# Performance work log

Measured on AMD Instinct MI355X. Metric: run time of the kernel, lower is better.

The kernel has to match this reference:

```python
import jax, jax.numpy as jnp
import numpy as np

N_LAYERS = 2
D_MODEL = 1024
D_INNER = 2 * D_MODEL
D_STATE = 16
D_CONV = 4
DT_RANK = D_MODEL // 16  # 64
B_SZ, L = 1, 2048
EPS = 1e-5


def layernorm(x, w, b):
    mu = jnp.mean(x, axis=-1, keepdims=True)
    var = jnp.mean(jnp.square(x - mu), axis=-1, keepdims=True)
    return (x - mu) * jax.lax.rsqrt(var + EPS) * w + b


def mamba(x, in_w, cw, cb, xp_w, dtp_w, dtp_b, A_log, Dp, out_w):
    # x: [B, L, D_MODEL]
    Bn, Ln, _ = x.shape
    xz = jnp.einsum('bld,ed->ble', x, in_w)          # [B,L,2*D_INNER]
    xc, z = jnp.split(xz, 2, axis=-1)
    # causal depthwise conv1d (kernel D_CONV)
    xp = jnp.pad(xc, ((0, 0), (D_CONV - 1, 0), (0, 0)))
    xc = sum(xp[:, k:k + Ln, :] * cw[:, k] for k in range(D_CONV)) + cb
    xc = jax.nn.silu(xc)
    dbl = jnp.einsum('ble,re->blr', xc, xp_w)        # [B,L,DT_RANK+2*D_STATE]
    dt, Bm, Cm = jnp.split(dbl, [DT_RANK, DT_RANK + D_STATE], axis=-1)
    dt = jax.nn.softplus(jnp.einsum('blr,er->ble', dt, dtp_w) + dtp_b)  # [B,L,E]
    A = -jnp.exp(A_log)                              # [E,N], strictly negative
    dA = jnp.exp(dt[..., None] * A)                  # [B,L,E,N]
    dBu = (dt * xc)[..., None] * Bm[:, :, None, :]   # [B,L,E,N]

    def step(h, inp):
        dA_t, dBu_t, C_t = inp
        h = dA_t * h + dBu_t                         # [B,E,N]
        y = jnp.einsum('ben,bn->be', h, C_t)
        return h, y

    h0 = jnp.zeros((Bn, D_INNER, D_STATE), dA.dtype)
    _, ys = jax.lax.scan(step, h0, (dA.transpose(1, 0, 2, 3),
                                    dBu.transpose(1, 0, 2, 3),
                                    Cm.transpose(1, 0, 2)))
    y = ys.transpose(1, 0, 2) + xc * Dp              # [B,L,E]
    y = y * jax.nn.silu(z)
    return jnp.einsum('ble,de->bld', y, out_w)       # [B,L,D_MODEL]


def setup_inputs() -> dict:
    key = jax.random.key(0)
    ks = jax.random.split(key, 12)
    s = 0.02
    dt_init = np.log(np.expm1(0.01)).astype(np.float32)  # softplus^-1(0.01)
    A_row = jnp.log(jnp.arange(1, D_STATE + 1, dtype=jnp.float32))
    return {
        'x': jax.random.normal(ks[0], (B_SZ, L, D_MODEL), jnp.float32),
        'ln_w': jnp.ones((N_LAYERS, D_MODEL), jnp.float32),
        'ln_b': jnp.zeros((N_LAYERS, D_MODEL), jnp.float32),
        'in_proj_w': jax.random.normal(ks[1], (N_LAYERS, 2 * D_INNER, D_MODEL)) * s,
        'conv_w': jax.random.normal(ks[2], (N_LAYERS, D_INNER, D_CONV)) * 0.2,
        'conv_b': jnp.zeros((N_LAYERS, D_INNER), jnp.float32),
        'x_proj_w': jax.random.normal(ks[3], (N_LAYERS, DT_RANK + 2 * D_STATE, D_INNER)) * s,
        'dt_proj_w': jax.random.normal(ks[4], (N_LAYERS, D_INNER, DT_RANK)) * (DT_RANK ** -0.5),
        'dt_proj_b': jnp.full((N_LAYERS, D_INNER), dt_init),
        'A_log': jnp.broadcast_to(A_row, (N_LAYERS, D_INNER, D_STATE)).copy(),
        'D_skip': jnp.ones((N_LAYERS, D_INNER), jnp.float32),
        'out_proj_w': jax.random.normal(ks[5], (N_LAYERS, D_MODEL, D_INNER)) * s,
        'norm_f_w': jnp.ones((D_MODEL,), jnp.float32),
        'norm_f_b': jnp.zeros((D_MODEL,), jnp.float32),
    }


def reference(x, ln_w, ln_b, in_proj_w, conv_w, conv_b, x_proj_w, dt_proj_w,
              dt_proj_b, A_log, D_skip, out_proj_w, norm_f_w, norm_f_b):
    for i in range(N_LAYERS):
        h = layernorm(x, ln_w[i], ln_b[i])
        h = mamba(h, in_proj_w[i], conv_w[i], conv_b[i], x_proj_w[i],
                  dt_proj_w[i], dt_proj_b[i], A_log[i], D_skip[i], out_proj_w[i])
        x = h + x  # residual (dropout/drop_path are identity in eval)
    return layernorm(x, norm_f_w, norm_f_b)
```

## Files before the change

### kernel.cpp

```cpp
#include <hip/hip_runtime.h>
#include <hip/hip_bf16.h>
#include <math.h>

#define LSEQ 2048
#define DMODEL 1024
#define DINNER 2048
#define DSTATE 16
#define DCONV 4
#define DTRANK 64
#define RPROJ 96

#define CHUNK 16
#define NCHUNK (LSEQ / CHUNK)

#define XSPLIT 4

typedef __attribute__((ext_vector_type(8))) short bf16x8;
typedef __attribute__((ext_vector_type(4))) float f32x4;

__device__ __forceinline__ float softplusf(float x) {
    return (x > 20.f) ? x : log1pf(__expf(x));
}
__device__ __forceinline__ float siluf(float x) {
    return x / (1.f + __expf(-x));
}
__device__ __forceinline__ short f2bf(float f) {
    union { float f; unsigned u; } v; v.f = f;
    unsigned r = v.u + 0x7FFFu + ((v.u >> 16) & 1u);
    return (short)(r >> 16);
}
__device__ __forceinline__ float bf2f(short h) {
    union { unsigned u; float f; } v;
    v.u = ((unsigned)(unsigned short)h) << 16;
    return v.f;
}

__device__ __forceinline__ void cvt8(const float* __restrict__ s,
                                     short* __restrict__ d, int i) {
    const float4 a = *(const float4*)(s + i);
    const float4 b = *(const float4*)(s + i + 4);
    alignas(16) short h[8];
    h[0] = f2bf(a.x); h[1] = f2bf(a.y); h[2] = f2bf(a.z); h[3] = f2bf(a.w);
    h[4] = f2bf(b.x); h[5] = f2bf(b.y); h[6] = f2bf(b.z); h[7] = f2bf(b.w);
    *(uint4*)(d + i) = *(const uint4*)h;
}

__global__ __launch_bounds__(256) void cvt_weights(
    const float* __restrict__ s0, short* __restrict__ d0, int n0,
    const float* __restrict__ s1, short* __restrict__ d1, int n1,
    const float* __restrict__ s2, short* __restrict__ d2, int n2,
    const float* __restrict__ s3, short* __restrict__ d3, int n3)
{
    int i = (blockIdx.x * 256 + threadIdx.x) * 8;
    if (i < n0) { cvt8(s0, d0, i); return; }
    i -= n0;
    if (i < n1) { cvt8(s1, d1, i); return; }
    i -= n1;
    if (i < n2) { cvt8(s2, d2, i); return; }
    i -= n2;
    if (i < n3) { cvt8(s3, d3, i); return; }
}

__global__ __launch_bounds__(256) void ln_kernel(
    const float* __restrict__ x, const float* __restrict__ w,
    const float* __restrict__ b, float* __restrict__ outf,
    short* __restrict__ outb)
{
    __shared__ float s1[256], s2[256];
    const int row = blockIdx.x;
    const int tid = threadIdx.x;
    const float* xr = x + (size_t)row * DMODEL;
    float v[4];
    float s = 0.f, sq = 0.f;
#pragma unroll
    for (int k = 0; k < 4; k++) {
        v[k] = xr[k * 256 + tid];
        s += v[k];
        sq += v[k] * v[k];
    }
    s1[tid] = s; s2[tid] = sq;
    __syncthreads();
    for (int off = 128; off > 0; off >>= 1) {
        if (tid < off) { s1[tid] += s1[tid + off]; s2[tid] += s2[tid + off]; }
        __syncthreads();
    }
    const float mu = s1[0] * (1.f / DMODEL);
    const float var = s2[0] * (1.f / DMODEL) - mu * mu;
    const float rstd = rsqrtf(var + 1e-5f);
#pragma unroll
    for (int k = 0; k < 4; k++) {
        const int i = k * 256 + tid;
        const float o = (v[k] - mu) * rstd * w[i] + b[i];
        if (outf) outf[(size_t)row * DMODEL + i] = o;
        if (outb) outb[(size_t)row * DMODEL + i] = f2bf(o);
    }
}

template<int MI, int NJ, int MODE>
__global__ __launch_bounds__(256) void gemm_mfma(
    const short* __restrict__ A, int lda,
    const short* __restrict__ W, int ldw,
    float* __restrict__ Cf, short* __restrict__ Cb, int ldc,
    int M, int N, int K,
    const float* __restrict__ resid)
{
    constexpr int BM = 32 * MI;
    constexpr int BN = 32 * NJ;
    constexpr int AISS = BM / 64;
    constexpr int WISS = BN / 64;
    __shared__ alignas(16) short As[BM * 32];
    __shared__ alignas(16) short Ws[BN * 32];

    const int tid = threadIdx.x;
    const int lane = tid & 63;
    const int w = tid >> 6;
    const int wr = w >> 1, wc = w & 1;
    const int row0 = blockIdx.y * BM;
    const int col0 = blockIdx.x * BN;
    const int kbeg = blockIdx.z * K;

    const int srow = tid >> 2;
    const int skch = ((tid & 3) ^ ((srow >> 1) & 3)) * 8;

    f32x4 acc[MI][NJ];
#pragma unroll
    for (int i = 0; i < MI; i++)
#pragma unroll
        for (int j = 0; j < NJ; j++) acc[i][j] = (f32x4)0.f;

    const int lrow = lane & 15;
    const int q = lane >> 4;

    for (int kt = kbeg; kt < kbeg + K; kt += 32) {
        __syncthreads();
#pragma unroll
        for (int j = 0; j < AISS; j++) {
            const short* gp = A + (size_t)(row0 + j * 64 + srow) * lda + kt + skch;
            __builtin_amdgcn_global_load_lds(
                (const __attribute__((address_space(1))) void*)gp,
                (__attribute__((address_space(3))) void*)(&As[j * 2048 + tid * 8]),
                16, 0, 0);
        }
#pragma unroll
        for (int j = 0; j < WISS; j++) {
            const int wrow = col0 + j * 64 + srow;
            if (wrow < N) {
                const short* gp = W + (size_t)wrow * ldw + kt + skch;
                __builtin_amdgcn_global_load_lds(
                    (const __attribute__((address_space(1))) void*)gp,
                    (__attribute__((address_space(3))) void*)(&Ws[j * 2048 + tid * 8]),
                    16, 0, 0);
            }
        }
        __syncthreads();

        bf16x8 af[MI], bfr[NJ];
#pragma unroll
        for (int i = 0; i < MI; i++) {
            const int R = wr * (16 * MI) + i * 16 + lrow;
            af[i] = *(const bf16x8*)&As[R * 32 + ((q ^ ((R >> 1) & 3)) * 8)];
        }
#pragma unroll
        for (int j = 0; j < NJ; j++) {
            const int R = wc * (16 * NJ) + j * 16 + lrow;
            bfr[j] = *(const bf16x8*)&Ws[R * 32 + ((q ^ ((R >> 1) & 3)) * 8)];
        }
#pragma unroll
        for (int i = 0; i < MI; i++)
#pragma unroll
            for (int j = 0; j < NJ; j++)
                acc[i][j] = __builtin_amdgcn_mfma_f32_16x16x32_bf16(
                    af[i], bfr[j], acc[i][j], 0, 0, 0);
    }

    const int rbase = row0 + wr * (16 * MI);
    const int cbase = col0 + wc * (16 * NJ);
#pragma unroll
    for (int i = 0; i < MI; i++) {
#pragma unroll
        for (int j = 0; j < NJ; j++) {
            const int gcol = cbase + j * 16 + lrow;
            if (gcol < N) {
#pragma unroll
                for (int r = 0; r < 4; r++) {
                    const int grow = rbase + i * 16 + (lane >> 4) * 4 + r;
                    float v = acc[i][j][r];
                    if (MODE == 2) {
                        Cf[(size_t)grow * ldc + gcol] =
                            v + resid[(size_t)grow * ldc + gcol];
                    } else if (MODE == 3) {
                        Cb[(size_t)grow * ldc + gcol] = f2bf(v);
                    } else {
                        atomicAdd(&Cf[(size_t)grow * ldc + gcol], v);
                    }
                }
            }
        }
    }
}

__global__ __launch_bounds__(256) void dtproj_kernel(
    const float* __restrict__ dbl,
    const short* __restrict__ dtp_w,
    const float* __restrict__ dtp_b,
    short* __restrict__ dt_bf)
{
    __shared__ alignas(16) short As[64 * 32];
    __shared__ alignas(16) short Ws[128 * 32];
    const int tid = threadIdx.x;
    const int lane = tid & 63;
    const int w = tid >> 6;
    const int wr = w >> 1, wc = w & 1;
    const int row0 = blockIdx.y * 64;
    const int col0 = blockIdx.x * 128;
    const int srow = tid >> 2;
    const int skch = ((tid & 3) ^ ((srow >> 1) & 3)) * 8;
    const int lrow = lane & 15;
    const int q = lane >> 4;

    f32x4 acc[2][4];
#pragma unroll
    for (int i = 0; i < 2; i++)
#pragma unroll
        for (int j = 0; j < 4; j++) acc[i][j] = (f32x4)0.f;

#pragma unroll
    for (int kt = 0; kt < 64; kt += 32) {
        __syncthreads();
        {
            const float* gp = dbl + (size_t)(row0 + srow) * RPROJ + kt + skch;
            const float4 a = *(const float4*)gp;
            const float4 b = *(const float4*)(gp + 4);
            alignas(16) short h[8];
            h[0] = f2bf(a.x); h[1] = f2bf(a.y); h[2] = f2bf(a.z); h[3] = f2bf(a.w);
            h[4] = f2bf(b.x); h[5] = f2bf(b.y); h[6] = f2bf(b.z); h[7] = f2bf(b.w);
            *(uint4*)(As + tid * 8) = *(const uint4*)h;
        }
#pragma unroll
        for (int j = 0; j < 2; j++) {
            const short* gp = dtp_w + (size_t)(col0 + j * 64 + srow) * DTRANK + kt + skch;
            __builtin_amdgcn_global_load_lds(
                (const __attribute__((address_space(1))) void*)gp,
                (__attribute__((address_space(3))) void*)(&Ws[j * 2048 + tid * 8]),
                16, 0, 0);
        }
        __syncthreads();

        bf16x8 af[2], bfr[4];
#pragma unroll
        for (int i = 0; i < 2; i++) {
            const int R = wr * 32 + i * 16 + lrow;
            af[i] = *(const bf16x8*)&As[R * 32 + ((q ^ ((R >> 1) & 3)) * 8)];
        }
#pragma unroll
        for (int j = 0; j < 4; j++) {
            const int R = wc * 64 + j * 16 + lrow;
            bfr[j] = *(const bf16x8*)&Ws[R * 32 + ((q ^ ((R >> 1) & 3)) * 8)];
        }
#pragma unroll
        for (int i = 0; i < 2; i++)
#pragma unroll
            for (int j = 0; j < 4; j++)
                acc[i][j] = __builtin_amdgcn_mfma_f32_16x16x32_bf16(
                    af[i], bfr[j], acc[i][j], 0, 0, 0);
    }

    const int rbase = row0 + wr * 32;
    const int cbase = col0 + wc * 64;
#pragma unroll
    for (int i = 0; i < 2; i++)
#pragma unroll
        for (int j = 0; j < 4; j++) {
            const int gcol = cbase + j * 16 + lrow;
#pragma unroll
            for (int r = 0; r < 4; r++) {
                const int grow = rbase + i * 16 + (lane >> 4) * 4 + r;
                dt_bf[(size_t)grow * DINNER + gcol] =
                    f2bf(softplusf(acc[i][j][r] + dtp_b[gcol]));
            }
        }
}

__global__ __launch_bounds__(256) void conv_silu_kernel(
    const short* __restrict__ xzb, const float* __restrict__ cw,
    const float* __restrict__ cb, short* __restrict__ xcb,
    float* __restrict__ dbl_zero)
{
    const int g = blockIdx.x * 256 + threadIdx.x;
    if (g < (LSEQ * RPROJ) / 4)
        *(float4*)(dbl_zero + g * 4) = make_float4(0.f, 0.f, 0.f, 0.f);
    const int t = g >> 8;
    const int c0 = (g & 255) * 8;
    float acc[8];
#pragma unroll
    for (int j = 0; j < 8; j++) acc[j] = cb[c0 + j];
#pragma unroll
    for (int k = 0; k < DCONV; k++) {
        const int tt = t - (DCONV - 1) + k;
        if (tt >= 0) {
            const bf16x8 v = *(const bf16x8*)(xzb + (size_t)tt * (2 * DINNER) + c0);
#pragma unroll
            for (int j = 0; j < 8; j++)
                acc[j] += bf2f(v[j]) * cw[(c0 + j) * DCONV + k];
        }
    }
    alignas(16) short h[8];
#pragma unroll
    for (int j = 0; j < 8; j++) h[j] = f2bf(siluf(acc[j]));
    *(uint4*)(xcb + (size_t)t * DINNER + c0) = *(const uint4*)h;
}

__global__ __launch_bounds__(256) void scan_pass1(
    const short* __restrict__ dtb,
    const short* __restrict__ xcb,
    const float* __restrict__ dbl,
    const float* __restrict__ A_log,
    float* __restrict__ S,
    float* __restrict__ sumdt)
{
    const int e = blockIdx.x * 256 + threadIdx.x;
    const int c = blockIdx.y;
    float a[DSTATE];
#pragma unroll
    for (int n = 0; n < DSTATE; n++) a[n] = -__expf(A_log[(size_t)e * DSTATE + n]);
    float h[DSTATE];
#pragma unroll
    for (int n = 0; n < DSTATE; n++) h[n] = 0.f;
    float sd = 0.f;

    __shared__ float sBC[CHUNK][32];
    for (int i = threadIdx.x; i < CHUNK * 32; i += 256) {
        const int tl = i >> 5, j = i & 31;
        sBC[tl][j] = dbl[(size_t)(c * CHUNK + tl) * RPROJ + DTRANK + j];
    }
    __syncthreads();

    const size_t rb = (size_t)c * CHUNK * DINNER + e;
    short dt_c = dtb[rb], xc_c = xcb[rb];
#pragma unroll
    for (int tl = 0; tl < CHUNK; tl++) {
        short dt_n = 0, xc_n = 0;
        if (tl + 1 < CHUNK) {
            dt_n = dtb[rb + (size_t)(tl + 1) * DINNER];
            xc_n = xcb[rb + (size_t)(tl + 1) * DINNER];
        }
        const float dtv = bf2f(dt_c);
        const float du = dtv * bf2f(xc_c);
        sd += dtv;
#pragma unroll
        for (int n = 0; n < DSTATE; n++) {
            const float dA = __expf(dtv * a[n]);
            h[n] = dA * h[n] + du * sBC[tl][n];
        }
        dt_c = dt_n; xc_c = xc_n;
    }
    sumdt[(size_t)c * DINNER + e] = sd;
#pragma unroll
    for (int n = 0; n < DSTATE; n++)
        S[((size_t)c * DSTATE + n) * DINNER + e] = h[n];
}

__global__ __launch_bounds__(256) void scan_pass2(
    const float* __restrict__ A_log,
    const float* __restrict__ sumdt,
    float* __restrict__ S)
{
    const int idx = blockIdx.x * 256 + threadIdx.x;
    const int e = idx & (DINNER - 1);
    const int n = idx >> 11;
    const float a = -__expf(A_log[(size_t)e * DSTATE + n]);
    const size_t base = (size_t)n * DINNER + e;
    const size_t cstr = (size_t)DSTATE * DINNER;
    float H = 0.f;
    float sc = S[base];
    float sd = sumdt[e];
    for (int c = 0; c < NCHUNK; c++) {
        float sc_n = 0.f, sd_n = 0.f;
        if (c + 1 < NCHUNK) {
            sc_n = S[base + (size_t)(c + 1) * cstr];
            sd_n = sumdt[(size_t)(c + 1) * DINNER + e];
        }
        S[base + (size_t)c * cstr] = H;
        H = __expf(a * sd) * H + sc;
        sc = sc_n; sd = sd_n;
    }
}

__global__ __launch_bounds__(256) void scan_pass3(
    const short* __restrict__ dtb,
    const short* __restrict__ xcb,
    const float* __restrict__ dbl,
    const short* __restrict__ xzb,
    const float* __restrict__ A_log,
    const float* __restrict__ Dp,
    const float* __restrict__ S,
    short* __restrict__ yb)
{
    const int e = blockIdx.x * 256 + threadIdx.x;
    const int c = blockIdx.y;
    float a[DSTATE];
#pragma unroll
    for (int n = 0; n < DSTATE; n++) a[n] = -__expf(A_log[(size_t)e * DSTATE + n]);
    float h[DSTATE];
#pragma unroll
    for (int n = 0; n < DSTATE; n++)
        h[n] = S[((size_t)c * DSTATE + n) * DINNER + e];
    const float dskip = Dp[e];

    __shared__ float sBC[CHUNK][32];
    for (int i = threadIdx.x; i < CHUNK * 32; i += 256) {
        const int tl = i >> 5, j = i & 31;
        sBC[tl][j] = dbl[(size_t)(c * CHUNK + tl) * RPROJ + DTRANK + j];
    }
    __syncthreads();

    const size_t rb = (size_t)c * CHUNK * DINNER + e;
    const size_t zb = (size_t)c * CHUNK * (2 * DINNER) + DINNER + e;
    short dt_c = dtb[rb], xc_c = xcb[rb], z_c = xzb[zb];
#pragma unroll
    for (int tl = 0; tl < CHUNK; tl++) {
        short dt_n = 0, xc_n = 0, z_n = 0;
        if (tl + 1 < CHUNK) {
            dt_n = dtb[rb + (size_t)(tl + 1) * DINNER];
            xc_n = xcb[rb + (size_t)(tl + 1) * DINNER];
            z_n = xzb[zb + (size_t)(tl + 1) * (2 * DINNER)];
        }
        const float dtv = bf2f(dt_c);
        const float xcv = bf2f(xc_c);
        const float du = dtv * xcv;
        float yv = 0.f;
#pragma unroll
        for (int n = 0; n < DSTATE; n++) {
            const float dA = __expf(dtv * a[n]);
            h[n] = dA * h[n] + du * sBC[tl][n];
            yv += h[n] * sBC[tl][16 + n];
        }
        yv = (yv + xcv * dskip) * siluf(bf2f(z_c));
        yb[rb + (size_t)tl * DINNER] = f2bf(yv);
        dt_c = dt_n; xc_c = xc_n; z_c = z_n;
    }
}

extern "C" void kernel_launch(void* const* d_in, const int* in_sizes, int n_in,
                              void* d_out, int out_size, void* d_ws, size_t ws_size,
                              hipStream_t stream) {
    const float* x_in   = (const float*)d_in[0];
    const float* ln_w   = (const float*)d_in[1];
    const float* ln_b   = (const float*)d_in[2];
    const float* in_w   = (const float*)d_in[3];
    const float* conv_w = (const float*)d_in[4];
    const float* conv_b = (const float*)d_in[5];
    const float* xp_w   = (const float*)d_in[6];
    const float* dtp_w  = (const float*)d_in[7];
    const float* dtp_b  = (const float*)d_in[8];
    const float* A_log  = (const float*)d_in[9];
    const float* D_skip = (const float*)d_in[10];
    const float* out_w  = (const float*)d_in[11];
    const float* nf_w   = (const float*)d_in[12];
    const float* nf_b   = (const float*)d_in[13];
    float* out = (float*)d_out;

    float* w = (float*)d_ws;
    float* buf_x = w; w += (size_t)LSEQ * DMODEL;
    float* dbl   = w; w += (size_t)LSEQ * RPROJ;
    float* Sbuf  = w; w += (size_t)NCHUNK * DSTATE * DINNER;
    float* sumdt = w; w += (size_t)NCHUNK * DINNER;
    short* h_bf    = (short*)w; w += (size_t)LSEQ * DMODEL / 2;
    short* xz_bf   = (short*)w; w += (size_t)LSEQ * 2 * DINNER / 2;
    short* xc_bf   = (short*)w; w += (size_t)LSEQ * DINNER / 2;
    short* dt_bf   = (short*)w; w += (size_t)LSEQ * DINNER / 2;
    short* y_bf    = (short*)w; w += (size_t)LSEQ * DINNER / 2;
    short* in_w_bf  = (short*)w; w += (size_t)2 * (2 * DINNER) * DMODEL / 2;
    short* xp_w_bf  = (short*)w; w += (size_t)2 * RPROJ * DINNER / 2;
    short* dtp_w_bf = (short*)w; w += (size_t)2 * DINNER * DTRANK / 2;
    short* out_w_bf = (short*)w; w += (size_t)2 * DMODEL * DINNER / 2;

    {
        const int n1 = 2 * (2 * DINNER) * DMODEL;
        const int n2 = 2 * RPROJ * DINNER;
        const int n3 = 2 * DMODEL * DINNER;
        const int n4 = 2 * DINNER * DTRANK;
        const int total = n1 + n2 + n3 + n4;
        cvt_weights<<<dim3(total / (256 * 8)), dim3(256), 0, stream>>>(
            in_w, in_w_bf, n1, xp_w, xp_w_bf, n2,
            out_w, out_w_bf, n3, dtp_w, dtp_w_bf, n4);
    }

    for (int layer = 0; layer < 2; layer++) {
        const float* resid_src = (layer == 0) ? x_in : buf_x;
        ln_kernel<<<dim3(LSEQ), dim3(256), 0, stream>>>(
            resid_src, ln_w + layer * DMODEL, ln_b + layer * DMODEL,
            nullptr, h_bf);
        gemm_mfma<4, 4, 3><<<dim3((2 * DINNER) / 128, LSEQ / 128), dim3(256), 0, stream>>>(
            h_bf, DMODEL, in_w_bf + (size_t)layer * 2 * DINNER * DMODEL, DMODEL,
            nullptr, xz_bf, 2 * DINNER, LSEQ, 2 * DINNER, DMODEL, nullptr);
        conv_silu_kernel<<<dim3((LSEQ * DINNER / 8) / 256), dim3(256), 0, stream>>>(
            xz_bf, conv_w + (size_t)layer * DINNER * DCONV, conv_b + layer * DINNER,
            xc_bf, dbl);
        gemm_mfma<2, 2, 6><<<dim3(2, LSEQ / 64, XSPLIT), dim3(256), 0, stream>>>(
            xc_bf, DINNER, xp_w_bf + (size_t)layer * RPROJ * DINNER, DINNER,
            dbl, nullptr, RPROJ, LSEQ, RPROJ, DINNER / XSPLIT, nullptr);
        dtproj_kernel<<<dim3(DINNER / 128, LSEQ / 64), dim3(256), 0, stream>>>(
            dbl, dtp_w_bf + (size_t)layer * DINNER * DTRANK,
            dtp_b + layer * DINNER, dt_bf);
        const float* Al = A_log + (size_t)layer * DINNER * DSTATE;
        scan_pass1<<<dim3(DINNER / 256, NCHUNK), dim3(256), 0, stream>>>(
            dt_bf, xc_bf, dbl, Al, Sbuf, sumdt);
        scan_pass2<<<dim3((DINNER * DSTATE) / 256), dim3(256), 0, stream>>>(
            Al, sumdt, Sbuf);
        scan_pass3<<<dim3(DINNER / 256, NCHUNK), dim3(256), 0, stream>>>(
            dt_bf, xc_bf, dbl, xz_bf, Al, D_skip + layer * DINNER, Sbuf, y_bf);
        gemm_mfma<2, 2, 2><<<dim3(DMODEL / 64, LSEQ / 64), dim3(256), 0, stream>>>(
            y_bf, DINNER, out_w_bf + (size_t)layer * DMODEL * DINNER, DINNER,
            buf_x, nullptr, DMODEL, LSEQ, DMODEL, DINNER, resid_src);
    }
    ln_kernel<<<dim3(LSEQ), dim3(256), 0, stream>>>(buf_x, nf_w, nf_b, out, nullptr);
}
```

Measured before the change: 458.9 us.

## Double GEMM K-tile to 64 with 8-way swizzle, enlarge out_proj tile, unroll scan pass2

The MFMA GEMM now stages 64-wide K slices in LDS using a new XOR swizzle over 8 chunks. This halves the number of barrier pairs per K and issues two MFMA k-steps per stage. The out_proj GEMM uses a 128x64 block tile for more reuse per load, at the cost of more accumulators per thread and fewer blocks. scan_pass2 is unrolled by four so loads are issued ahead of the serial recurrence.

```diff
diff --git a/kernel.cpp b/kernel.cpp
--- a/kernel.cpp
+++ b/kernel.cpp
@@ -106,10 +106,10 @@
 {
     constexpr int BM = 32 * MI;
     constexpr int BN = 32 * NJ;
-    constexpr int AISS = BM / 64;
-    constexpr int WISS = BN / 64;
-    __shared__ alignas(16) short As[BM * 32];
-    __shared__ alignas(16) short Ws[BN * 32];
+    constexpr int AISS = BM / 32;
+    constexpr int WISS = BN / 32;
+    __shared__ alignas(16) short As[BM * 64];
+    __shared__ alignas(16) short Ws[BN * 64];
 
     const int tid = threadIdx.x;
     const int lane = tid & 63;
@@ -119,8 +119,9 @@
     const int col0 = blockIdx.x * BN;
     const int kbeg = blockIdx.z * K;
 
-    const int srow = tid >> 2;
-    const int skch = ((tid & 3) ^ ((srow >> 1) & 3)) * 8;
+    const int srow = tid >> 3;
+    const int dch  = tid & 7;
+    const int skch = (dch ^ (srow & 7)) * 8;
 
     f32x4 acc[MI][NJ];
 #pragma unroll
@@ -131,11 +132,11 @@
     const int lrow = lane & 15;
     const int q = lane >> 4;
 
-    for (int kt = kbeg; kt < kbeg + K; kt += 32) {
+    for (int kt = kbeg; kt < kbeg + K; kt += 64) {
         __syncthreads();
 #pragma unroll
         for (int j = 0; j < AISS; j++) {
-            const short* gp = A + (size_t)(row0 + j * 64 + srow) * lda + kt + skch;
+            const short* gp = A + (size_t)(row0 + j * 32 + srow) * lda + kt + skch;
             __builtin_amdgcn_global_load_lds(
                 (const __attribute__((address_space(1))) void*)gp,
                 (__attribute__((address_space(3))) void*)(&As[j * 2048 + tid * 8]),
@@ -143,7 +144,7 @@
         }
 #pragma unroll
         for (int j = 0; j < WISS; j++) {
-            const int wrow = col0 + j * 64 + srow;
+            const int wrow = col0 + j * 32 + srow;
             if (wrow < N) {
                 const short* gp = W + (size_t)wrow * ldw + kt + skch;
                 __builtin_amdgcn_global_load_lds(
@@ -154,23 +155,28 @@
         }
         __syncthreads();
 
-        bf16x8 af[MI], bfr[NJ];
-#pragma unroll
-        for (int i = 0; i < MI; i++) {
-            const int R = wr * (16 * MI) + i * 16 + lrow;
-            af[i] = *(const bf16x8*)&As[R * 32 + ((q ^ ((R >> 1) & 3)) * 8)];
-        }
-#pragma unroll
-        for (int j = 0; j < NJ; j++) {
-            const int R = wc * (16 * NJ) + j * 16 + lrow;
-            bfr[j] = *(const bf16x8*)&Ws[R * 32 + ((q ^ ((R >> 1) & 3)) * 8)];
-        }
-#pragma unroll
-        for (int i = 0; i < MI; i++)
-#pragma unroll
-            for (int j = 0; j < NJ; j++)
-                acc[i][j] = __builtin_amdgcn_mfma_f32_16x16x32_bf16(
-                    af[i], bfr[j], acc[i][j], 0, 0, 0);
+#pragma unroll
+        for (int ks = 0; ks < 2; ks++) {
+            bf16x8 af[MI], bfr[NJ];
+#pragma unroll
+            for (int i = 0; i < MI; i++) {
+                const int R = wr * (16 * MI) + i * 16 + lrow;
+                const int pc = (ks * 4 + q) ^ (R & 7);
+                af[i] = *(const bf16x8*)&As[R * 64 + pc * 8];
+            }
+#pragma unroll
+            for (int j = 0; j < NJ; j++) {
+                const int R = wc * (16 * NJ) + j * 16 + lrow;
+                const int pc = (ks * 4 + q) ^ (R & 7);
+                bfr[j] = *(const bf16x8*)&Ws[R * 64 + pc * 8];
+            }
+#pragma unroll
+            for (int i = 0; i < MI; i++)
+#pragma unroll
+                for (int j = 0; j < NJ; j++)
+                    acc[i][j] = __builtin_amdgcn_mfma_f32_16x16x32_bf16(
+                        af[i], bfr[j], acc[i][j], 0, 0, 0);
+        }
     }
 
     const int rbase = row0 + wr * (16 * MI);
@@ -372,17 +378,23 @@
     const size_t base = (size_t)n * DINNER + e;
     const size_t cstr = (size_t)DSTATE * DINNER;
     float H = 0.f;
-    float sc = S[base];
-    float sd = sumdt[e];
-    for (int c = 0; c < NCHUNK; c++) {
-        float sc_n = 0.f, sd_n = 0.f;
-        if (c + 1 < NCHUNK) {
-            sc_n = S[base + (size_t)(c + 1) * cstr];
-            sd_n = sumdt[(size_t)(c + 1) * DINNER + e];
-        }
-        S[base + (size_t)c * cstr] = H;
-        H = __expf(a * sd) * H + sc;
-        sc = sc_n; sd = sd_n;
+    for (int c = 0; c < NCHUNK; c += 4) {
+        const float sc0 = S[base + (size_t)(c + 0) * cstr];
+        const float sc1 = S[base + (size_t)(c + 1) * cstr];
+        const float sc2 = S[base + (size_t)(c + 2) * cstr];
+        const float sc3 = S[base + (size_t)(c + 3) * cstr];
+        const float sd0 = sumdt[(size_t)(c + 0) * DINNER + e];
+        const float sd1 = sumdt[(size_t)(c + 1) * DINNER + e];
+        const float sd2 = sumdt[(size_t)(c + 2) * DINNER + e];
+        const float sd3 = sumdt[(size_t)(c + 3) * DINNER + e];
+        S[base + (size_t)(c + 0) * cstr] = H;
+        H = __expf(a * sd0) * H + sc0;
+        S[base + (size_t)(c + 1) * cstr] = H;
+        H = __expf(a * sd1) * H + sc1;
+        S[base + (size_t)(c + 2) * cstr] = H;
+        H = __expf(a * sd2) * H + sc2;
+        S[base + (size_t)(c + 3) * cstr] = H;
+        H = __expf(a * sd3) * H + sc3;
     }
 }
 
@@ -510,7 +522,7 @@
             Al, sumdt, Sbuf);
         scan_pass3<<<dim3(DINNER / 256, NCHUNK), dim3(256), 0, stream>>>(
             dt_bf, xc_bf, dbl, xz_bf, Al, D_skip + layer * DINNER, Sbuf, y_bf);
-        gemm_mfma<2, 2, 2><<<dim3(DMODEL / 64, LSEQ / 64), dim3(256), 0, stream>>>(
+        gemm_mfma<4, 2, 2><<<dim3(DMODEL / 64, LSEQ / 128), dim3(256), 0, stream>>>(
             y_bf, DINNER, out_w_bf + (size_t)layer * DMODEL * DINNER, DINNER,
             buf_x, nullptr, DMODEL, LSEQ, DMODEL, DINNER, resid_src);
     }
```

New measurement: 456.9 us. No clear change (-0.4%).
